# Optimization experiments

Measured on AMD Instinct MI355X. Metric: run time of the kernel, lower is better.

The kernel has to match this reference:

```python
import jax, jax.numpy as jnp
import numpy as np

D_MODEL = 256
D_FFN = 1024
N_LEVELS = 4
N_HEADS = 8
N_POINTS = 4
HEAD_DIM = D_MODEL // N_HEADS
SPATIAL = [(128, 128), (64, 64), (32, 32), (16, 16)]
LQ = sum(h * w for h, w in SPATIAL)  # 21760
B = 2


def setup_inputs() -> dict:
    key = jax.random.key(0)
    ks = jax.random.split(key, 24)

    def w(k, shape, s=0.02):
        return (jax.random.normal(k, shape) * s).astype(jnp.float32)

    HLP = N_HEADS * N_LEVELS * N_POINTS
    starts = np.cumsum([0] + [h * w_ for h, w_ in SPATIAL[:-1]])
    return {
        "src": jax.random.normal(ks[0], (B, LQ, D_MODEL), jnp.float32),
        "pos": 0.1 * jax.random.normal(ks[1], (B, LQ, D_MODEL), jnp.float32),
        "reference_points": jax.random.uniform(ks[2], (B, LQ, N_LEVELS, 2), jnp.float32),
        "W_off": w(ks[3], (D_MODEL, HLP * 2)),
        "b_off": w(ks[4], (HLP * 2,), 0.5),
        "W_attn": w(ks[5], (D_MODEL, HLP)),
        "b_attn": jnp.zeros((HLP,), jnp.float32),
        "W_val": w(ks[6], (D_MODEL, D_MODEL)),
        "b_val": jnp.zeros((D_MODEL,), jnp.float32),
        "W_out": w(ks[7], (D_MODEL, D_MODEL)),
        "b_out": jnp.zeros((D_MODEL,), jnp.float32),
        "ln1_g": jnp.ones((D_MODEL,), jnp.float32),
        "ln1_b": jnp.zeros((D_MODEL,), jnp.float32),
        "W1": w(ks[8], (D_MODEL, D_FFN)),
        "b1": jnp.zeros((D_FFN,), jnp.float32),
        "W2": w(ks[9], (D_FFN, D_MODEL)),
        "b2": jnp.zeros((D_MODEL,), jnp.float32),
        "ln2_g": jnp.ones((D_MODEL,), jnp.float32),
        "ln2_b": jnp.zeros((D_MODEL,), jnp.float32),
        "spatial_shapes": np.array(SPATIAL, np.int32),
        "level_start_index": np.array(starts, np.int32),
    }


def _layernorm(x, g, b):
    mu = x.mean(-1, keepdims=True)
    var = ((x - mu) ** 2).mean(-1, keepdims=True)
    return (x - mu) * jax.lax.rsqrt(var + 1e-5) * g + b


def _bilinear_sample(v, x, y, H, W):
    # v: [N, H, W, D]; x, y: [N, Lq, P] pixel coords (align_corners=False, zero pad)
    x0f = jnp.floor(x)
    y0f = jnp.floor(y)
    x0 = x0f.astype(jnp.int32)
    y0 = y0f.astype(jnp.int32)
    wx1 = x - x0f
    wy1 = y - y0f
    wx0 = 1.0 - wx1
    wy0 = 1.0 - wy1
    vf = v.reshape(v.shape[0], H * W, v.shape[-1])

    def gather(xi, yi, wt):
        valid = (xi >= 0) & (xi < W) & (yi >= 0) & (yi < H)
        idx = jnp.clip(yi, 0, H - 1) * W + jnp.clip(xi, 0, W - 1)
        g = jnp.take_along_axis(vf, idx.reshape(idx.shape[0], -1)[..., None], axis=1)
        g = g.reshape(*xi.shape, vf.shape[-1])
        return g * (wt * valid.astype(wt.dtype))[..., None]

    return (gather(x0, y0, wx0 * wy0) + gather(x0 + 1, y0, wx1 * wy0)
            + gather(x0, y0 + 1, wx0 * wy1) + gather(x0 + 1, y0 + 1, wx1 * wy1))


def _ms_deform_attn(query, src, reference_points, W_off, b_off, W_attn, b_attn,
                    W_val, b_val, W_out, b_out, spatial_shapes):
    Bq, Lq, _ = query.shape
    ss = np.asarray(spatial_shapes)
    value = (src @ W_val + b_val).reshape(Bq, Lq, N_HEADS, HEAD_DIM)
    off = (query @ W_off + b_off).reshape(Bq, Lq, N_HEADS, N_LEVELS, N_POINTS, 2)
    attn = (query @ W_attn + b_attn).reshape(Bq, Lq, N_HEADS, N_LEVELS * N_POINTS)
    attn = jax.nn.softmax(attn, axis=-1).reshape(Bq, Lq, N_HEADS, N_LEVELS, N_POINTS)
    # offset normalizer = (W, H) per level
    normalizer = jnp.asarray(ss[:, ::-1].astype(np.float32))  # [L, 2]
    loc = reference_points[:, :, None, :, None, :] + off / normalizer[None, None, None, :, None, :]
    # loc: [B, Lq, M, L, P, 2] normalized in [0,1]
    out = jnp.zeros((Bq, N_HEADS, Lq, HEAD_DIM), query.dtype)
    start = 0
    for lvl in range(N_LEVELS):
        H, W = int(ss[lvl, 0]), int(ss[lvl, 1])
        v = value[:, start:start + H * W]                                 # [B, HW, M, D]
        v = v.transpose(0, 2, 1, 3).reshape(Bq * N_HEADS, H, W, HEAD_DIM)
        l = loc[:, :, :, lvl]                                             # [B, Lq, M, P, 2]
        x = (l[..., 0] * W - 0.5).transpose(0, 2, 1, 3).reshape(Bq * N_HEADS, Lq, N_POINTS)
        y = (l[..., 1] * H - 0.5).transpose(0, 2, 1, 3).reshape(Bq * N_HEADS, Lq, N_POINTS)
        sampled = _bilinear_sample(v, x, y, H, W)                         # [BM, Lq, P, D]
        wgt = attn[:, :, :, lvl].transpose(0, 2, 1, 3).reshape(Bq * N_HEADS, Lq, N_POINTS)
        out = out + (sampled * wgt[..., None]).sum(2).reshape(Bq, N_HEADS, Lq, HEAD_DIM)
        start += H * W
    out = out.transpose(0, 2, 1, 3).reshape(Bq, Lq, D_MODEL)
    return out @ W_out + b_out


def reference(src, pos, reference_points, W_off, b_off, W_attn, b_attn, W_val, b_val,
              W_out, b_out, ln1_g, ln1_b, W1, b1, W2, b2, ln2_g, ln2_b,
              spatial_shapes, level_start_index):
    query = src + pos
    src2 = _ms_deform_attn(query, src, reference_points, W_off, b_off, W_attn, b_attn,
                           W_val, b_val, W_out, b_out, spatial_shapes)
    h = _layernorm(src + src2, ln1_g, ln1_b)
    ffn = jax.nn.relu(h @ W1 + b1) @ W2 + b2
    return _layernorm(h + ffn, ln2_g, ln2_b)
```

## Files before the change

kernel.cpp:

```cpp
#include <hip/hip_runtime.h>

typedef __bf16 bf16x8 __attribute__((ext_vector_type(8)));
typedef float f32x4 __attribute__((ext_vector_type(4)));

static constexpr int TOKS = 43520;
static constexpr int LQN  = 21760;

__device__ __forceinline__ unsigned short f2bf(float f) {
  union { float f; unsigned u; } v; v.f = f;
  return (unsigned short)((v.u + 0x7fffu + ((v.u >> 16) & 1u)) >> 16);
}
__device__ __forceinline__ float bf2f(unsigned short b) {
  union { unsigned u; float f; } v; v.u = ((unsigned)b) << 16; return v.f;
}

__global__ __launch_bounds__(256) void prewt_kernel(
    const float* __restrict__ src, const float* __restrict__ pos,
    unsigned short* __restrict__ srcb, unsigned short* __restrict__ qb,
    const float* __restrict__ W_val, const float* __restrict__ W_off,
    const float* __restrict__ W_attn, const float* __restrict__ W_out,
    const float* __restrict__ W1, const float* __restrict__ W2,
    const float* __restrict__ b_off, const float* __restrict__ b_attn,
    unsigned short* __restrict__ Wt_val, unsigned short* __restrict__ Wt_oa,
    unsigned short* __restrict__ Wt_out,
    unsigned short* __restrict__ Wt_1, unsigned short* __restrict__ Wt_2,
    float* __restrict__ b_oa) {
  const int bid = blockIdx.x;
  if (bid < 10880) {
    int i = bid * 256 + threadIdx.x;
    float4 s = ((const float4*)src)[i], p = ((const float4*)pos)[i];
    ((ushort4*)srcb)[i] = make_ushort4(f2bf(s.x), f2bf(s.y), f2bf(s.z), f2bf(s.w));
    ((ushort4*)qb)[i]   = make_ushort4(f2bf(s.x + p.x), f2bf(s.y + p.y),
                                       f2bf(s.z + p.z), f2bf(s.w + p.w));
    return;
  }
  int gid = (bid - 10880) * 256 + threadIdx.x;
  if (gid >= 754048) return;
  if (gid >= 753664) {
    int i = gid - 753664;
    b_oa[i] = (i < 256) ? b_off[i] : b_attn[i - 256];
    return;
  }
  const float* W; unsigned short* Wt; int idx, K, nsh;
  if (gid < 65536)       { W = W_val;  Wt = Wt_val;          idx = gid;          K = 256;  nsh = 8;  }
  else if (gid < 131072) { W = W_off;  Wt = Wt_oa;           idx = gid - 65536;  K = 256;  nsh = 8;  }
  else if (gid < 163840) { W = W_attn; Wt = Wt_oa + 65536;   idx = gid - 131072; K = 256;  nsh = 7;  }
  else if (gid < 229376) { W = W_out;  Wt = Wt_out;          idx = gid - 163840; K = 256;  nsh = 8;  }
  else if (gid < 491520) { W = W1;     Wt = Wt_1;            idx = gid - 229376; K = 256;  nsh = 10; }
  else                   { W = W2;     Wt = Wt_2;            idx = gid - 491520; K = 1024; nsh = 8;  }
  int k = idx >> nsh, n = idx & ((1 << nsh) - 1);
  Wt[n * K + k] = f2bf(W[idx]);
}

template <int K, int OUTOP>
__device__ __forceinline__ void gemm_body(unsigned short* __restrict__ As,
                                          unsigned short* __restrict__ Bs,
                                          const unsigned short* __restrict__ A,
                                          const unsigned short* __restrict__ Bt,
                                          const float* __restrict__ bias,
                                          const unsigned short* __restrict__ res,
                                          unsigned short* __restrict__ Cp,
                                          int N, int bm, int bn) {
  const int t = threadIdx.x;
  const int wave = t >> 6, lane = t & 63;
  const int wm = (wave & 1) << 6, wn = (wave >> 1) << 6;
  const int lr = lane & 15, lq = lane >> 4;
  const int row0 = t >> 2, cb0 = (t & 3) << 3;
  f32x4 acc[4][4] = {};
  const unsigned short* ga = A  + (size_t)(bm * 128 + row0) * K + cb0;
  const unsigned short* gb = Bt + (size_t)(bn * 128 + row0) * K + cb0;
  const size_t gs = (size_t)64 * K;
  uint4 pa0 = *(const uint4*)ga;
  uint4 pa1 = *(const uint4*)(ga + gs);
  uint4 pb0 = *(const uint4*)gb;
  uint4 pb1 = *(const uint4*)(gb + gs);
  int p = 0;
#pragma unroll 1
  for (int k0 = 0; k0 < K; k0 += 32) {
    unsigned short* Ab = As + p * 5120;
    unsigned short* Bb = Bs + p * 5120;
    *(uint4*)&Ab[row0 * 40 + cb0] = pa0;
    *(uint4*)&Ab[(row0 + 64) * 40 + cb0] = pa1;
    *(uint4*)&Bb[row0 * 40 + cb0] = pb0;
    *(uint4*)&Bb[(row0 + 64) * 40 + cb0] = pb1;
    __syncthreads();
    if (k0 + 32 < K) {
      pa0 = *(const uint4*)(ga + k0 + 32);
      pa1 = *(const uint4*)(ga + gs + k0 + 32);
      pb0 = *(const uint4*)(gb + k0 + 32);
      pb1 = *(const uint4*)(gb + gs + k0 + 32);
    }
    bf16x8 af[4], bfr[4];
#pragma unroll
    for (int i = 0; i < 4; i++) af[i] = *(const bf16x8*)&Ab[(wm + i * 16 + lr) * 40 + lq * 8];
#pragma unroll
    for (int j = 0; j < 4; j++) bfr[j] = *(const bf16x8*)&Bb[(wn + j * 16 + lr) * 40 + lq * 8];
#pragma unroll
    for (int i = 0; i < 4; i++)
#pragma unroll
      for (int j = 0; j < 4; j++)
        acc[i][j] = __builtin_amdgcn_mfma_f32_16x16x32_bf16(af[i], bfr[j], acc[i][j], 0, 0, 0);
    p ^= 1;
  }
  const int rb = bm * 128 + wm + lq * 4;
  const int cbase = bn * 128 + wn + lr;
#pragma unroll
  for (int j = 0; j < 4; j++) {
    const int col = cbase + j * 16;
    const float bv = bias[col];
#pragma unroll
    for (int i = 0; i < 4; i++) {
#pragma unroll
      for (int r = 0; r < 4; r++) {
        float v = acc[i][j][r] + bv;
        size_t o = (size_t)(rb + i * 16 + r) * N + col;
        if (OUTOP == 1) Cp[o] = f2bf(v);
        else if (OUTOP == 2) Cp[o] = f2bf(fmaxf(v, 0.f));
        else Cp[o] = f2bf(v + bf2f(res[o]));
      }
    }
  }
}

__global__ __launch_bounds__(256) void proj_kernel(
    const unsigned short* __restrict__ srcb, const unsigned short* __restrict__ qb,
    const unsigned short* __restrict__ Wt_val, const unsigned short* __restrict__ Wt_oa,
    const float* __restrict__ b_val, const float* __restrict__ b_oa,
    unsigned short* __restrict__ valb, unsigned short* __restrict__ oab) {
  __shared__ unsigned short As[2 * 5120];
  __shared__ unsigned short Bs[2 * 5120];
  const int bn = blockIdx.y;
  if (bn < 2)
    gemm_body<256, 1>(As, Bs, srcb, Wt_val, b_val, nullptr, valb, 256, blockIdx.x, bn);
  else
    gemm_body<256, 1>(As, Bs, qb, Wt_oa, b_oa, nullptr, oab, 384, blockIdx.x, bn - 2);
}

__global__ __launch_bounds__(256) void gemm_out_kernel(
    const unsigned short* __restrict__ A, const unsigned short* __restrict__ Bt,
    const float* __restrict__ bias, const unsigned short* __restrict__ res,
    unsigned short* __restrict__ C) {
  __shared__ unsigned short As[2 * 5120];
  __shared__ unsigned short Bs[2 * 5120];
  gemm_body<256, 3>(As, Bs, A, Bt, bias, res, C, 256, blockIdx.x, blockIdx.y);
}

__global__ __launch_bounds__(256) void gemm_ffn1_kernel(
    const unsigned short* __restrict__ A, const unsigned short* __restrict__ Bt,
    const float* __restrict__ bias, unsigned short* __restrict__ C) {
  __shared__ unsigned short As[2 * 5120];
  __shared__ unsigned short Bs[2 * 5120];
  gemm_body<256, 2>(As, Bs, A, Bt, bias, nullptr, C, 1024, blockIdx.x, blockIdx.y);
}

__global__ __launch_bounds__(256) void gemm_ffn2_kernel(
    const unsigned short* __restrict__ A, const unsigned short* __restrict__ Bt,
    const float* __restrict__ bias, const unsigned short* __restrict__ res,
    unsigned short* __restrict__ C) {
  __shared__ unsigned short As[2 * 5120];
  __shared__ unsigned short Bs[2 * 5120];
  gemm_body<1024, 3>(As, Bs, A, Bt, bias, res, C, 256, blockIdx.x, blockIdx.y);
}

__device__ __forceinline__ void fma8(uint4 v, float w, float* a) {
  const unsigned uu[4] = {v.x, v.y, v.z, v.w};
#pragma unroll
  for (int i = 0; i < 4; i++) {
    union { unsigned u; float f; } lo, hi;
    lo.u = uu[i] << 16;
    hi.u = uu[i] & 0xffff0000u;
    a[2 * i]     += w * lo.f;
    a[2 * i + 1] += w * hi.f;
  }
}

__global__ __launch_bounds__(256) void deform_kernel(const unsigned short* __restrict__ valb,
                                                     const unsigned short* __restrict__ oab,
                                                     const float* __restrict__ refp,
                                                     unsigned short* __restrict__ outb) {
  __shared__ float4 sW[8][8][17];
  __shared__ int4   sI[8][8][17];
  const int t = threadIdx.x;
  const int bid = blockIdx.x;
  const int nb = (bid & 7) * 680 + (bid >> 3);
  const int tok0 = nb * 8;

  {
    const int g = t >> 5, h = (t >> 2) & 7, l = t & 3;
    const int tok = tok0 + g;
    const unsigned short* lg = oab + (size_t)tok * 384 + 256 + h * 16;
    uint4 lv0 = ((const uint4*)lg)[0];
    uint4 lv1 = ((const uint4*)lg)[1];
    const unsigned lw[8] = {lv0.x, lv0.y, lv0.z, lv0.w, lv1.x, lv1.y, lv1.z, lv1.w};
    float w[16];
#pragma unroll
    for (int i = 0; i < 8; i++) {
      union { unsigned u; float f; } lo, hi;
      lo.u = lw[i] << 16; hi.u = lw[i] & 0xffff0000u;
      w[2 * i] = lo.f; w[2 * i + 1] = hi.f;
    }
    float mx = -1e30f;
#pragma unroll
    for (int i = 0; i < 16; i++) mx = fmaxf(mx, w[i]);
    float s = 0.f;
#pragma unroll
    for (int i = 0; i < 16; i++) { w[i] = __expf(w[i] - mx); s += w[i]; }
    const float inv = 1.f / s;
    uint4 ov = *(const uint4*)(oab + (size_t)tok * 384 + h * 32 + l * 8);
    const unsigned owv[4] = {ov.x, ov.y, ov.z, ov.w};
    float off[8];
#pragma unroll
    for (int i = 0; i < 4; i++) {
      union { unsigned u; float f; } lo, hi;
      lo.u = owv[i] << 16; hi.u = owv[i] & 0xffff0000u;
      off[2 * i] = lo.f; off[2 * i + 1] = hi.f;
    }
    const float* rp = refp + (size_t)tok * 8 + l * 2;
    const int S = 128 >> l;
    const float Sf = (float)S;
    const float rx = rp[0] * Sf - 0.5f;
    const float ry = rp[1] * Sf - 0.5f;
#pragma unroll
    for (int p = 0; p < 4; p++) {
      const int idx = l * 4 + p;
      const float x = rx + off[p * 2 + 0];
      const float y = ry + off[p * 2 + 1];
      const float aw = w[idx] * inv;
      const float x0f = floorf(x), y0f = floorf(y);
      const int x0 = (int)x0f, y0 = (int)y0f;
      const float fx = x - x0f, fy = y - y0f;
      const bool xin0 = (x0 >= 0) & (x0 < S), xin1 = (x0 + 1 >= 0) & (x0 + 1 < S);
      const bool yin0 = (y0 >= 0) & (y0 < S), yin1 = (y0 + 1 >= 0) & (y0 + 1 < S);
      const int xc0 = min(max(x0, 0), S - 1), xc1 = min(max(x0 + 1, 0), S - 1);
      const int yc0 = min(max(y0, 0), S - 1), yc1 = min(max(y0 + 1, 0), S - 1);
      sW[g][h][idx] = make_float4(aw * (1.f - fx) * (1.f - fy) * (float)(xin0 & yin0),
                                  aw * fx * (1.f - fy)         * (float)(xin1 & yin0),
                                  aw * (1.f - fx) * fy         * (float)(xin0 & yin1),
                                  aw * fx * fy                 * (float)(xin1 & yin1));
      sI[g][h][idx] = make_int4((yc0 * S + xc0) << 9, (yc0 * S + xc1) << 9,
                                (yc1 * S + xc0) << 9, (yc1 * S + xc1) << 9);
    }
  }
  __syncthreads();

  const int g = t >> 5, h = (t >> 2) & 7, dc = t & 3;
  const int tok = tok0 + g;
  const int b = tok / LQN;
  float acc[8] = {0.f, 0.f, 0.f, 0.f, 0.f, 0.f, 0.f, 0.f};
  const int ST[4] = {0, 16384, 20480, 21504};
#pragma unroll
  for (int l = 0; l < 4; l++) {
    const char* vbc = (const char*)(valb + ((size_t)(b * LQN + ST[l])) * 256 + h * 32 + dc * 8);
#pragma unroll
    for (int p = 0; p < 4; p++) {
      float4 W4 = sW[g][h][l * 4 + p];
      int4   I4 = sI[g][h][l * 4 + p];
      uint4 v00 = *(const uint4*)(vbc + I4.x);
      uint4 v10 = *(const uint4*)(vbc + I4.y);
      uint4 v01 = *(const uint4*)(vbc + I4.z);
      uint4 v11 = *(const uint4*)(vbc + I4.w);
      fma8(v00, W4.x, acc);
      fma8(v10, W4.y, acc);
      fma8(v01, W4.z, acc);
      fma8(v11, W4.w, acc);
    }
  }
  unsigned o[4];
#pragma unroll
  for (int i = 0; i < 4; i++)
    o[i] = (unsigned)f2bf(acc[2 * i]) | ((unsigned)f2bf(acc[2 * i + 1]) << 16);
  *(uint4*)(outb + (size_t)tok * 256 + h * 32 + dc * 8) = make_uint4(o[0], o[1], o[2], o[3]);
}

template <int OUT_F32>
__global__ __launch_bounds__(256) void ln_kernel(const ushort4* __restrict__ in,
                                                 const float* __restrict__ g,
                                                 const float* __restrict__ beta,
                                                 void* __restrict__ outp) {
  const int wv = blockIdx.x * 4 + (threadIdx.x >> 6);
  const int lane = threadIdx.x & 63;
  const size_t idx = (size_t)wv * 64 + lane;
  ushort4 u = in[idx];
  float x0 = bf2f(u.x), x1 = bf2f(u.y), x2 = bf2f(u.z), x3 = bf2f(u.w);
  float sum = x0 + x1 + x2 + x3;
#pragma unroll
  for (int o = 32; o >= 1; o >>= 1) sum += __shfl_xor(sum, o, 64);
  const float mu = sum * (1.f / 256.f);
  float d0 = x0 - mu, d1 = x1 - mu, d2 = x2 - mu, d3 = x3 - mu;
  float ss = d0 * d0 + d1 * d1 + d2 * d2 + d3 * d3;
#pragma unroll
  for (int o = 32; o >= 1; o >>= 1) ss += __shfl_xor(ss, o, 64);
  const float rs = rsqrtf(ss * (1.f / 256.f) + 1e-5f);
  float4 gg = ((const float4*)g)[lane], bb = ((const float4*)beta)[lane];
  float y0 = d0 * rs * gg.x + bb.x;
  float y1 = d1 * rs * gg.y + bb.y;
  float y2 = d2 * rs * gg.z + bb.z;
  float y3 = d3 * rs * gg.w + bb.w;
  if (OUT_F32) ((float4*)outp)[idx] = make_float4(y0, y1, y2, y3);
  else ((ushort4*)outp)[idx] = make_ushort4(f2bf(y0), f2bf(y1), f2bf(y2), f2bf(y3));
}

extern "C" void kernel_launch(void* const* d_in, const int* in_sizes, int n_in,
                              void* d_out, int out_size, void* d_ws, size_t ws_size,
                              hipStream_t stream) {
  (void)in_sizes; (void)n_in; (void)out_size; (void)ws_size;
  const float* src    = (const float*)d_in[0];
  const float* pos    = (const float*)d_in[1];
  const float* refp   = (const float*)d_in[2];
  const float* W_off  = (const float*)d_in[3];
  const float* b_off  = (const float*)d_in[4];
  const float* W_attn = (const float*)d_in[5];
  const float* b_attn = (const float*)d_in[6];
  const float* W_val  = (const float*)d_in[7];
  const float* b_val  = (const float*)d_in[8];
  const float* W_out  = (const float*)d_in[9];
  const float* b_out  = (const float*)d_in[10];
  const float* ln1_g  = (const float*)d_in[11];
  const float* ln1_b  = (const float*)d_in[12];
  const float* W1     = (const float*)d_in[13];
  const float* b1     = (const float*)d_in[14];
  const float* W2     = (const float*)d_in[15];
  const float* b2     = (const float*)d_in[16];
  const float* ln2_g  = (const float*)d_in[17];
  const float* ln2_b  = (const float*)d_in[18];

  char* ws = (char*)d_ws;
  unsigned short* Wt_val = (unsigned short*)ws;
  unsigned short* Wt_oa  = Wt_val + 65536;
  unsigned short* Wt_out = Wt_oa + 98304;
  unsigned short* Wt_1   = Wt_out + 65536;
  unsigned short* Wt_2   = Wt_1 + 262144;
  float*          b_oa   = (float*)(Wt_2 + 262144);
  const size_t WPOOL = 2u * 1024 * 1024;

  const size_t SZ_bf = (size_t)TOKS * 256 * 2;
  const size_t SZ_oa = (size_t)TOKS * 384 * 2;

  unsigned short* srcb = (unsigned short*)(ws + WPOOL);
  unsigned short* qb   = (unsigned short*)(ws + WPOOL + SZ_bf);
  unsigned short* valb = (unsigned short*)(ws + WPOOL + 2 * SZ_bf);
  unsigned short* oab  = (unsigned short*)(ws + WPOOL + 3 * SZ_bf);
  unsigned short* h_bf = (unsigned short*)(ws + WPOOL + 3 * SZ_bf + SZ_oa);
  unsigned short* hb   = (unsigned short*)(ws + WPOOL + 3 * SZ_bf + SZ_oa + SZ_bf);
  unsigned short* attnoutb = qb;
  unsigned short* preLN1b  = valb;
  unsigned short* preLN2b  = valb;

  prewt_kernel<<<13826, 256, 0, stream>>>(src, pos, srcb, qb,
                                          W_val, W_off, W_attn, W_out, W1, W2, b_off, b_attn,
                                          Wt_val, Wt_oa, Wt_out, Wt_1, Wt_2, b_oa);

  proj_kernel<<<dim3(340, 5), 256, 0, stream>>>(srcb, qb, Wt_val, Wt_oa, b_val, b_oa,
                                                valb, oab);

  deform_kernel<<<TOKS / 8, 256, 0, stream>>>(valb, oab, refp, attnoutb);

  gemm_out_kernel<<<dim3(340, 2), 256, 0, stream>>>(attnoutb, Wt_out, b_out, srcb, preLN1b);
  ln_kernel<0><<<10880, 256, 0, stream>>>((const ushort4*)preLN1b, ln1_g, ln1_b, h_bf);

  gemm_ffn1_kernel<<<dim3(340, 8), 256, 0, stream>>>(h_bf, Wt_1, b1, hb);
  gemm_ffn2_kernel<<<dim3(340, 2), 256, 0, stream>>>(hb, Wt_2, b2, h_bf, preLN2b);

  ln_kernel<1><<<10880, 256, 0, stream>>>((const ushort4*)preLN2b, ln2_g, ln2_b, d_out);
}
```

Before: 437.4 us.

## Stream GEMM tiles with direct global-to-LDS loads and swizzle; compress deform indices

```diff
diff --git a/kernel.cpp b/kernel.cpp
--- a/kernel.cpp
+++ b/kernel.cpp
@@ -12,6 +12,12 @@
 }
 __device__ __forceinline__ float bf2f(unsigned short b) {
   union { unsigned u; float f; } v; v.u = ((unsigned)b) << 16; return v.f;
+}
+
+__device__ __forceinline__ void gload16(const unsigned short* g, unsigned short* l) {
+  __builtin_amdgcn_global_load_lds((const __attribute__((address_space(1))) unsigned int*)g,
+                                   (__attribute__((address_space(3))) unsigned int*)l,
+                                   16, 0, 0);
 }
 
 __global__ __launch_bounds__(256) void prewt_kernel(
@@ -65,41 +71,47 @@
   const int wave = t >> 6, lane = t & 63;
   const int wm = (wave & 1) << 6, wn = (wave >> 1) << 6;
   const int lr = lane & 15, lq = lane >> 4;
-  const int row0 = t >> 2, cb0 = (t & 3) << 3;
+  const int cA = (lq ^ (lr & 3)) * 8;
+  const int srow = t >> 2;
+  const int scol = ((t & 3) ^ (srow & 3)) * 8;
+  const unsigned short* gsA = A  + (size_t)(bm * 128 + srow) * K + scol;
+  const unsigned short* gsB = Bt + (size_t)(bn * 128 + srow) * K + scol;
+  const size_t gstep = (size_t)64 * K;
   f32x4 acc[4][4] = {};
-  const unsigned short* ga = A  + (size_t)(bm * 128 + row0) * K + cb0;
-  const unsigned short* gb = Bt + (size_t)(bn * 128 + row0) * K + cb0;
-  const size_t gs = (size_t)64 * K;
-  uint4 pa0 = *(const uint4*)ga;
-  uint4 pa1 = *(const uint4*)(ga + gs);
-  uint4 pb0 = *(const uint4*)gb;
-  uint4 pb1 = *(const uint4*)(gb + gs);
+
+  {
+    unsigned short* Ad = As + wave * 512;
+    unsigned short* Bd = Bs + wave * 512;
+    gload16(gsA,         Ad);
+    gload16(gsA + gstep, Ad + 2048);
+    gload16(gsB,         Bd);
+    gload16(gsB + gstep, Bd + 2048);
+  }
+  __syncthreads();
   int p = 0;
-#pragma unroll 1
+#pragma unroll 2
   for (int k0 = 0; k0 < K; k0 += 32) {
-    unsigned short* Ab = As + p * 5120;
-    unsigned short* Bb = Bs + p * 5120;
-    *(uint4*)&Ab[row0 * 40 + cb0] = pa0;
-    *(uint4*)&Ab[(row0 + 64) * 40 + cb0] = pa1;
-    *(uint4*)&Bb[row0 * 40 + cb0] = pb0;
-    *(uint4*)&Bb[(row0 + 64) * 40 + cb0] = pb1;
-    __syncthreads();
     if (k0 + 32 < K) {
-      pa0 = *(const uint4*)(ga + k0 + 32);
-      pa1 = *(const uint4*)(ga + gs + k0 + 32);
-      pb0 = *(const uint4*)(gb + k0 + 32);
-      pb1 = *(const uint4*)(gb + gs + k0 + 32);
-    }
+      unsigned short* Ad = As + (p ^ 1) * 4096 + wave * 512;
+      unsigned short* Bd = Bs + (p ^ 1) * 4096 + wave * 512;
+      gload16(gsA + k0 + 32,         Ad);
+      gload16(gsA + gstep + k0 + 32, Ad + 2048);
+      gload16(gsB + k0 + 32,         Bd);
+      gload16(gsB + gstep + k0 + 32, Bd + 2048);
+    }
+    const unsigned short* Ab = As + p * 4096;
+    const unsigned short* Bb = Bs + p * 4096;
     bf16x8 af[4], bfr[4];
 #pragma unroll
-    for (int i = 0; i < 4; i++) af[i] = *(const bf16x8*)&Ab[(wm + i * 16 + lr) * 40 + lq * 8];
-#pragma unroll
-    for (int j = 0; j < 4; j++) bfr[j] = *(const bf16x8*)&Bb[(wn + j * 16 + lr) * 40 + lq * 8];
+    for (int i = 0; i < 4; i++) af[i]  = *(const bf16x8*)&Ab[(wm + i * 16 + lr) * 32 + cA];
+#pragma unroll
+    for (int j = 0; j < 4; j++) bfr[j] = *(const bf16x8*)&Bb[(wn + j * 16 + lr) * 32 + cA];
 #pragma unroll
     for (int i = 0; i < 4; i++)
 #pragma unroll
       for (int j = 0; j < 4; j++)
         acc[i][j] = __builtin_amdgcn_mfma_f32_16x16x32_bf16(af[i], bfr[j], acc[i][j], 0, 0, 0);
+    __syncthreads();
     p ^= 1;
   }
   const int rb = bm * 128 + wm + lq * 4;
@@ -127,8 +139,8 @@
     const unsigned short* __restrict__ Wt_val, const unsigned short* __restrict__ Wt_oa,
     const float* __restrict__ b_val, const float* __restrict__ b_oa,
     unsigned short* __restrict__ valb, unsigned short* __restrict__ oab) {
-  __shared__ unsigned short As[2 * 5120];
-  __shared__ unsigned short Bs[2 * 5120];
+  __shared__ unsigned short As[2 * 4096];
+  __shared__ unsigned short Bs[2 * 4096];
   const int bn = blockIdx.y;
   if (bn < 2)
     gemm_body<256, 1>(As, Bs, srcb, Wt_val, b_val, nullptr, valb, 256, blockIdx.x, bn);
@@ -140,16 +152,16 @@
     const unsigned short* __restrict__ A, const unsigned short* __restrict__ Bt,
     const float* __restrict__ bias, const unsigned short* __restrict__ res,
     unsigned short* __restrict__ C) {
-  __shared__ unsigned short As[2 * 5120];
-  __shared__ unsigned short Bs[2 * 5120];
+  __shared__ unsigned short As[2 * 4096];
+  __shared__ unsigned short Bs[2 * 4096];
   gemm_body<256, 3>(As, Bs, A, Bt, bias, res, C, 256, blockIdx.x, blockIdx.y);
 }
 
 __global__ __launch_bounds__(256) void gemm_ffn1_kernel(
     const unsigned short* __restrict__ A, const unsigned short* __restrict__ Bt,
     const float* __restrict__ bias, unsigned short* __restrict__ C) {
-  __shared__ unsigned short As[2 * 5120];
-  __shared__ unsigned short Bs[2 * 5120];
+  __shared__ unsigned short As[2 * 4096];
+  __shared__ unsigned short Bs[2 * 4096];
   gemm_body<256, 2>(As, Bs, A, Bt, bias, nullptr, C, 1024, blockIdx.x, blockIdx.y);
 }
 
@@ -157,8 +169,8 @@
     const unsigned short* __restrict__ A, const unsigned short* __restrict__ Bt,
     const float* __restrict__ bias, const unsigned short* __restrict__ res,
     unsigned short* __restrict__ C) {
-  __shared__ unsigned short As[2 * 5120];
-  __shared__ unsigned short Bs[2 * 5120];
+  __shared__ unsigned short As[2 * 4096];
+  __shared__ unsigned short Bs[2 * 4096];
   gemm_body<1024, 3>(As, Bs, A, Bt, bias, res, C, 256, blockIdx.x, blockIdx.y);
 }
 
@@ -179,7 +191,7 @@
                                                      const float* __restrict__ refp,
                                                      unsigned short* __restrict__ outb) {
   __shared__ float4 sW[8][8][17];
-  __shared__ int4   sI[8][8][17];
+  __shared__ int2   sI[8][8][17];
   const int t = threadIdx.x;
   const int bid = blockIdx.x;
   const int nb = (bid & 7) * 680 + (bid >> 3);
@@ -237,8 +249,10 @@
                                   aw * fx * (1.f - fy)         * (float)(xin1 & yin0),
                                   aw * (1.f - fx) * fy         * (float)(xin0 & yin1),
                                   aw * fx * fy                 * (float)(xin1 & yin1));
-      sI[g][h][idx] = make_int4((yc0 * S + xc0) << 9, (yc0 * S + xc1) << 9,
-                                (yc1 * S + xc0) << 9, (yc1 * S + xc1) << 9);
+      const int base = (yc0 * S + xc0) << 9;
+      const int dx = (xc1 - xc0) << 9;
+      const int dy = ((yc1 - yc0) * S) << 9;
+      sI[g][h][idx] = make_int2(base, dy | (dx >> 9));
     }
   }
   __syncthreads();
@@ -254,11 +268,13 @@
 #pragma unroll
     for (int p = 0; p < 4; p++) {
       float4 W4 = sW[g][h][l * 4 + p];
-      int4   I4 = sI[g][h][l * 4 + p];
-      uint4 v00 = *(const uint4*)(vbc + I4.x);
-      uint4 v10 = *(const uint4*)(vbc + I4.y);
-      uint4 v01 = *(const uint4*)(vbc + I4.z);
-      uint4 v11 = *(const uint4*)(vbc + I4.w);
+      int2   I2 = sI[g][h][l * 4 + p];
+      const int dx = (I2.y & 1) << 9;
+      const int dy = I2.y & ~1;
+      uint4 v00 = *(const uint4*)(vbc + I2.x);
+      uint4 v10 = *(const uint4*)(vbc + I2.x + dx);
+      uint4 v01 = *(const uint4*)(vbc + I2.x + dy);
+      uint4 v11 = *(const uint4*)(vbc + I2.x + dy + dx);
       fma8(v00, W4.x, acc);
       fma8(v10, W4.y, acc);
       fma8(v01, W4.z, acc);
```

Measured after the change: 457.9 us. 4.7% more time.

## Fuse LayerNorm into out-proj and FFN2 GEMMs with 128x256 tiles

Applied to the files above, without the earlier changes.

```diff
diff --git a/kernel.cpp b/kernel.cpp
--- a/kernel.cpp
+++ b/kernel.cpp
@@ -136,30 +136,180 @@
     gemm_body<256, 1>(As, Bs, qb, Wt_oa, b_oa, nullptr, oab, 384, blockIdx.x, bn - 2);
 }
 
-__global__ __launch_bounds__(256) void gemm_out_kernel(
+template <int K, int MODE>
+__device__ __forceinline__ void big_body(unsigned short* __restrict__ As,
+                                         unsigned short* __restrict__ Bs,
+                                         const unsigned short* __restrict__ A,
+                                         const unsigned short* __restrict__ Bt,
+                                         const float* __restrict__ bias,
+                                         const unsigned short* __restrict__ res,
+                                         const float* __restrict__ gamma,
+                                         const float* __restrict__ beta,
+                                         void* __restrict__ outp,
+                                         int N, int bm, int bn) {
+  const int t = threadIdx.x;
+  const int wave = t >> 6, lane = t & 63;
+  const int wm = (wave & 1) << 6, wn = (wave >> 1) << 7;
+  const int lr = lane & 15, lq = lane >> 4;
+  const int row0 = t >> 2, cb0 = (t & 3) << 3;
+  f32x4 acc[4][8] = {};
+  const unsigned short* ga = A  + (size_t)(bm * 128 + row0) * K + cb0;
+  const unsigned short* gb = Bt + (size_t)(bn * 256 + row0) * K + cb0;
+  const size_t gs = (size_t)64 * K;
+  uint4 pa0 = *(const uint4*)ga;
+  uint4 pa1 = *(const uint4*)(ga + gs);
+  uint4 pb0 = *(const uint4*)gb;
+  uint4 pb1 = *(const uint4*)(gb + gs);
+  uint4 pb2 = *(const uint4*)(gb + 2 * gs);
+  uint4 pb3 = *(const uint4*)(gb + 3 * gs);
+  int p = 0;
+#pragma unroll 1
+  for (int k0 = 0; k0 < K; k0 += 32) {
+    unsigned short* Ab = As + p * 5120;
+    unsigned short* Bb = Bs + p * 10240;
+    *(uint4*)&Ab[row0 * 40 + cb0] = pa0;
+    *(uint4*)&Ab[(row0 + 64) * 40 + cb0] = pa1;
+    *(uint4*)&Bb[row0 * 40 + cb0] = pb0;
+    *(uint4*)&Bb[(row0 + 64) * 40 + cb0] = pb1;
+    *(uint4*)&Bb[(row0 + 128) * 40 + cb0] = pb2;
+    *(uint4*)&Bb[(row0 + 192) * 40 + cb0] = pb3;
+    __syncthreads();
+    if (k0 + 32 < K) {
+      pa0 = *(const uint4*)(ga + k0 + 32);
+      pa1 = *(const uint4*)(ga + gs + k0 + 32);
+      pb0 = *(const uint4*)(gb + k0 + 32);
+      pb1 = *(const uint4*)(gb + gs + k0 + 32);
+      pb2 = *(const uint4*)(gb + 2 * gs + k0 + 32);
+      pb3 = *(const uint4*)(gb + 3 * gs + k0 + 32);
+    }
+    bf16x8 af[4], bfr[8];
+#pragma unroll
+    for (int i = 0; i < 4; i++) af[i]  = *(const bf16x8*)&Ab[(wm + i * 16 + lr) * 40 + lq * 8];
+#pragma unroll
+    for (int j = 0; j < 8; j++) bfr[j] = *(const bf16x8*)&Bb[(wn + j * 16 + lr) * 40 + lq * 8];
+#pragma unroll
+    for (int i = 0; i < 4; i++)
+#pragma unroll
+      for (int j = 0; j < 8; j++)
+        acc[i][j] = __builtin_amdgcn_mfma_f32_16x16x32_bf16(af[i], bfr[j], acc[i][j], 0, 0, 0);
+    p ^= 1;
+  }
+  const int rb = bm * 128 + wm + lq * 4;
+  if (MODE == 0) {
+    const int cbase = bn * 256 + wn + lr;
+#pragma unroll
+    for (int j = 0; j < 8; j++) {
+      const int col = cbase + j * 16;
+      const float bv = bias[col];
+#pragma unroll
+      for (int i = 0; i < 4; i++)
+#pragma unroll
+        for (int r = 0; r < 4; r++) {
+          float v = acc[i][j][r] + bv;
+          ((unsigned short*)outp)[(size_t)(rb + i * 16 + r) * N + col] = f2bf(fmaxf(v, 0.f));
+        }
+    }
+    return;
+  }
+  __syncthreads();
+  float* red = (float*)As;
+  const int wnIdx = wave >> 1;
+  float vsum[4][4], vsq[4][4];
+#pragma unroll
+  for (int i = 0; i < 4; i++)
+#pragma unroll
+    for (int r = 0; r < 4; r++) { vsum[i][r] = 0.f; vsq[i][r] = 0.f; }
+#pragma unroll
+  for (int j = 0; j < 8; j++) {
+    const int col = wn + j * 16 + lr;
+    const float bv = bias[col];
+#pragma unroll
+    for (int i = 0; i < 4; i++)
+#pragma unroll
+      for (int r = 0; r < 4; r++) {
+        const int grow = rb + i * 16 + r;
+        float v = acc[i][j][r] + bv + bf2f(res[(size_t)grow * 256 + col]);
+        acc[i][j][r] = v;
+        vsum[i][r] += v;
+        vsq[i][r]  += v * v;
+      }
+  }
+#pragma unroll
+  for (int m = 1; m <= 8; m <<= 1)
+#pragma unroll
+    for (int i = 0; i < 4; i++)
+#pragma unroll
+      for (int r = 0; r < 4; r++) {
+        vsum[i][r] += __shfl_xor(vsum[i][r], m, 64);
+        vsq[i][r]  += __shfl_xor(vsq[i][r],  m, 64);
+      }
+  if (lr == 0) {
+#pragma unroll
+    for (int i = 0; i < 4; i++)
+#pragma unroll
+      for (int r = 0; r < 4; r++) {
+        const int lrow = wm + i * 16 + lq * 4 + r;
+        red[wnIdx * 128 + lrow]       = vsum[i][r];
+        red[256 + wnIdx * 128 + lrow] = vsq[i][r];
+      }
+  }
+  __syncthreads();
+  float mu[4][4], rstd[4][4];
+#pragma unroll
+  for (int i = 0; i < 4; i++)
+#pragma unroll
+    for (int r = 0; r < 4; r++) {
+      const int lrow = wm + i * 16 + lq * 4 + r;
+      const float ts = vsum[i][r] + red[(1 - wnIdx) * 128 + lrow];
+      const float tq = vsq[i][r]  + red[256 + (1 - wnIdx) * 128 + lrow];
+      const float m_ = ts * (1.f / 256.f);
+      float var = tq * (1.f / 256.f) - m_ * m_;
+      mu[i][r] = m_;
+      rstd[i][r] = rsqrtf(var + 1e-5f);
+    }
+#pragma unroll
+  for (int j = 0; j < 8; j++) {
+    const int col = wn + j * 16 + lr;
+    const float gg = gamma[col], bb = beta[col];
+#pragma unroll
+    for (int i = 0; i < 4; i++)
+#pragma unroll
+      for (int r = 0; r < 4; r++) {
+        const int grow = rb + i * 16 + r;
+        const float y = (acc[i][j][r] - mu[i][r]) * rstd[i][r] * gg + bb;
+        if (MODE == 1) ((unsigned short*)outp)[(size_t)grow * 256 + col] = f2bf(y);
+        else           ((float*)outp)[(size_t)grow * 256 + col] = y;
+      }
+  }
+}
+
+__global__ __launch_bounds__(256, 2) void out_ln_kernel(
     const unsigned short* __restrict__ A, const unsigned short* __restrict__ Bt,
     const float* __restrict__ bias, const unsigned short* __restrict__ res,
+    const float* __restrict__ gamma, const float* __restrict__ beta,
     unsigned short* __restrict__ C) {
   __shared__ unsigned short As[2 * 5120];
-  __shared__ unsigned short Bs[2 * 5120];
-  gemm_body<256, 3>(As, Bs, A, Bt, bias, res, C, 256, blockIdx.x, blockIdx.y);
-}
-
-__global__ __launch_bounds__(256) void gemm_ffn1_kernel(
+  __shared__ unsigned short Bs[2 * 10240];
+  big_body<256, 1>(As, Bs, A, Bt, bias, res, gamma, beta, C, 256, blockIdx.x, 0);
+}
+
+__global__ __launch_bounds__(256, 2) void ffn1_kernel(
     const unsigned short* __restrict__ A, const unsigned short* __restrict__ Bt,
     const float* __restrict__ bias, unsigned short* __restrict__ C) {
   __shared__ unsigned short As[2 * 5120];
-  __shared__ unsigned short Bs[2 * 5120];
-  gemm_body<256, 2>(As, Bs, A, Bt, bias, nullptr, C, 1024, blockIdx.x, blockIdx.y);
-}
-
-__global__ __launch_bounds__(256) void gemm_ffn2_kernel(
+  __shared__ unsigned short Bs[2 * 10240];
+  big_body<256, 0>(As, Bs, A, Bt, bias, nullptr, nullptr, nullptr, C, 1024,
+                   blockIdx.x, blockIdx.y);
+}
+
+__global__ __launch_bounds__(256, 2) void ffn2_ln_kernel(
     const unsigned short* __restrict__ A, const unsigned short* __restrict__ Bt,
     const float* __restrict__ bias, const unsigned short* __restrict__ res,
-    unsigned short* __restrict__ C) {
+    const float* __restrict__ gamma, const float* __restrict__ beta,
+    float* __restrict__ C) {
   __shared__ unsigned short As[2 * 5120];
-  __shared__ unsigned short Bs[2 * 5120];
-  gemm_body<1024, 3>(As, Bs, A, Bt, bias, res, C, 256, blockIdx.x, blockIdx.y);
+  __shared__ unsigned short Bs[2 * 10240];
+  big_body<1024, 2>(As, Bs, A, Bt, bias, res, gamma, beta, C, 256, blockIdx.x, 0);
 }
 
 __device__ __forceinline__ void fma8(uint4 v, float w, float* a) {
@@ -270,34 +420,6 @@
   for (int i = 0; i < 4; i++)
     o[i] = (unsigned)f2bf(acc[2 * i]) | ((unsigned)f2bf(acc[2 * i + 1]) << 16);
   *(uint4*)(outb + (size_t)tok * 256 + h * 32 + dc * 8) = make_uint4(o[0], o[1], o[2], o[3]);
-}
-
-template <int OUT_F32>
-__global__ __launch_bounds__(256) void ln_kernel(const ushort4* __restrict__ in,
-                                                 const float* __restrict__ g,
-                                                 const float* __restrict__ beta,
-                                                 void* __restrict__ outp) {
-  const int wv = blockIdx.x * 4 + (threadIdx.x >> 6);
-  const int lane = threadIdx.x & 63;
-  const size_t idx = (size_t)wv * 64 + lane;
-  ushort4 u = in[idx];
-  float x0 = bf2f(u.x), x1 = bf2f(u.y), x2 = bf2f(u.z), x3 = bf2f(u.w);
-  float sum = x0 + x1 + x2 + x3;
-#pragma unroll
-  for (int o = 32; o >= 1; o >>= 1) sum += __shfl_xor(sum, o, 64);
-  const float mu = sum * (1.f / 256.f);
-  float d0 = x0 - mu, d1 = x1 - mu, d2 = x2 - mu, d3 = x3 - mu;
-  float ss = d0 * d0 + d1 * d1 + d2 * d2 + d3 * d3;
-#pragma unroll
-  for (int o = 32; o >= 1; o >>= 1) ss += __shfl_xor(ss, o, 64);
-  const float rs = rsqrtf(ss * (1.f / 256.f) + 1e-5f);
-  float4 gg = ((const float4*)g)[lane], bb = ((const float4*)beta)[lane];
-  float y0 = d0 * rs * gg.x + bb.x;
-  float y1 = d1 * rs * gg.y + bb.y;
-  float y2 = d2 * rs * gg.z + bb.z;
-  float y3 = d3 * rs * gg.w + bb.w;
-  if (OUT_F32) ((float4*)outp)[idx] = make_float4(y0, y1, y2, y3);
-  else ((ushort4*)outp)[idx] = make_ushort4(f2bf(y0), f2bf(y1), f2bf(y2), f2bf(y3));
 }
 
 extern "C" void kernel_launch(void* const* d_in, const int* in_sizes, int n_in,
@@ -343,8 +465,6 @@
   unsigned short* h_bf = (unsigned short*)(ws + WPOOL + 3 * SZ_bf + SZ_oa);
   unsigned short* hb   = (unsigned short*)(ws + WPOOL + 3 * SZ_bf + SZ_oa + SZ_bf);
   unsigned short* attnoutb = qb;
-  unsigned short* preLN1b  = valb;
-  unsigned short* preLN2b  = valb;
 
   prewt_kernel<<<13826, 256, 0, stream>>>(src, pos, srcb, qb,
                                           W_val, W_off, W_attn, W_out, W1, W2, b_off, b_attn,
@@ -355,11 +475,9 @@
 
   deform_kernel<<<TOKS / 8, 256, 0, stream>>>(valb, oab, refp, attnoutb);
 
-  gemm_out_kernel<<<dim3(340, 2), 256, 0, stream>>>(attnoutb, Wt_out, b_out, srcb, preLN1b);
-  ln_kernel<0><<<10880, 256, 0, stream>>>((const ushort4*)preLN1b, ln1_g, ln1_b, h_bf);
-
-  gemm_ffn1_kernel<<<dim3(340, 8), 256, 0, stream>>>(h_bf, Wt_1, b1, hb);
-  gemm_ffn2_kernel<<<dim3(340, 2), 256, 0, stream>>>(hb, Wt_2, b2, h_bf, preLN2b);
-
-  ln_kernel<1><<<10880, 256, 0, stream>>>((const ushort4*)preLN2b, ln2_g, ln2_b, d_out);
-}
+  out_ln_kernel<<<340, 256, 0, stream>>>(attnoutb, Wt_out, b_out, srcb, ln1_g, ln1_b, h_bf);
+
+  ffn1_kernel<<<dim3(340, 4), 256, 0, stream>>>(h_bf, Wt_1, b1, hb);
+
+  ffn2_ln_kernel<<<340, 256, 0, stream>>>(hb, Wt_2, b2, h_bf, ln2_g, ln2_b, (float*)d_out);
+}
```

Result: no change. 437.0 us (-0.1%).
